# Optimization experiments

Hardware: AMD Instinct MI355X
Metric: run time of the kernel (lower is better)

The kernel has to match this reference:

```python
import jax, jax.numpy as jnp
import numpy as np

B, S, I, E, NH, HID, L = 32, 512, 64, 128, 8, 1024, 4
HD = E // NH
TEMP = 0.05
EPS_BN = 1e-5
EPS_LN = 1e-5


def _pe(seq_len, d_model):
    # sinusoidal positional encoding, matches PositionalEncoding buffer pe[:seq_len, 0, :]
    pos = jnp.arange(seq_len, dtype=jnp.float32)[:, None]
    div = jnp.exp(jnp.arange(0, d_model, 2, dtype=jnp.float32) * (-np.log(10000.0) / d_model))
    pe = jnp.zeros((seq_len, d_model), jnp.float32)
    pe = pe.at[:, 0::2].set(jnp.sin(pos * div))
    pe = pe.at[:, 1::2].set(jnp.cos(pos * div))
    return pe


def _bn(x, g, b, axis):
    # eval-mode BatchNorm1d with running_mean=0, running_var=1 (affine scale+shift)
    sh = [1] * x.ndim
    sh[axis] = -1
    return x * (g / jnp.sqrt(1.0 + EPS_BN)).reshape(sh) + b.reshape(sh)


def _ln(x, g, b):
    m = jnp.mean(x, axis=-1, keepdims=True)
    v = jnp.var(x, axis=-1, keepdims=True)
    return (x - m) / jnp.sqrt(v + EPS_LN) * g + b


def _layer(h, Wqkv, bqkv, Wo, bo, g1, b1, g2, b2, W1, bf1, W2, bf2):
    # h: (S, B, E); post-LN torch TransformerEncoderLayer, relu FFN
    s, b = h.shape[0], h.shape[1]
    qkv = h @ Wqkv + bqkv                                  # (S, B, 3E)
    q, k, v = jnp.split(qkv, 3, axis=-1)
    sp = lambda t: t.reshape(s, b, NH, HD).transpose(1, 2, 0, 3)  # (B, NH, S, HD)
    q, k, v = sp(q), sp(k), sp(v)
    att = jax.nn.softmax(jnp.einsum('bhqd,bhkd->bhqk', q, k) * (1.0 / np.sqrt(HD)), axis=-1)
    o = jnp.einsum('bhqk,bhkd->bhqd', att, v).transpose(2, 0, 1, 3).reshape(s, b, E)
    h = _ln(h + o @ Wo + bo, g1, b1)
    ff = jax.nn.relu(h @ W1 + bf1) @ W2 + bf2
    h = _ln(h + ff, g2, b2)
    return h, att.mean(axis=1)  # attn averaged over heads: (B, S, S)


def setup_inputs() -> dict:
    key = jax.random.key(0)
    ks = iter(jax.random.split(key, 64))
    r = lambda *sh: jax.random.normal(next(ks), sh, jnp.float32) * 0.02
    return dict(
        x=jax.random.normal(next(ks), (B, S, I), jnp.float32),
        Wt=r(I, E), bt=r(E),
        bn1_g=jnp.ones(E), bn1_b=jnp.zeros(E),
        bn2_g=jnp.ones(E), bn2_b=jnp.zeros(E),
        Wqkv=r(L, E, 3 * E), bqkv=r(L, 3 * E), Wo=r(L, E, E), bo=r(L, E),
        ln1_g=jnp.ones((L, E)), ln1_b=jnp.zeros((L, E)),
        ln2_g=jnp.ones((L, E)), ln2_b=jnp.zeros((L, E)),
        W1=r(L, E, HID), b1=r(L, HID), W2=r(L, HID, E), b2=r(L, E),
        bn3_g=jnp.ones(E), bn3_b=jnp.zeros(E),
        Wd=r(E, I), bd=r(I), bn4_g=jnp.ones(I), bn4_b=jnp.zeros(I),
        Ws=r(S, HID), bs=r(HID), bn5_g=jnp.ones(HID), bn5_b=jnp.zeros(HID),
        Wtext=r(1024, HID), btext=r(HID), lnT_g=jnp.ones(HID), lnT_b=jnp.zeros(HID),
        sensor_emb=jax.random.normal(next(ks), (I, 1024), jnp.float32),
    )


def reference(x, Wt, bt, bn1_g, bn1_b, bn2_g, bn2_b,
              Wqkv, bqkv, Wo, bo, ln1_g, ln1_b, ln2_g, ln2_b,
              W1, b1, W2, b2, bn3_g, bn3_b,
              Wd, bd, bn4_g, bn4_b, Ws, bs, bn5_g, bn5_b,
              Wtext, btext, lnT_g, lnT_b, sensor_emb):
    # trunk_net: Linear -> BN(E) -> PE -> BN(E)
    h = x @ Wt + bt                                  # (B, S, E)
    h = _bn(h.transpose(0, 2, 1), bn1_g, bn1_b, 1)   # (B, E, S)
    h = h.transpose(2, 0, 1)                         # (S, B, E)
    h = h + _pe(h.shape[0], E)[:, None, :]
    h = _bn(h.transpose(1, 2, 0), bn2_g, bn2_b, 1)   # (B, E, S)
    h = h.transpose(2, 0, 1)                         # (S, B, E)
    for i in range(L):
        h, attn = _layer(h, Wqkv[i], bqkv[i], Wo[i], bo[i],
                         ln1_g[i], ln1_b[i], ln2_g[i], ln2_b[i],
                         W1[i], b1[i], W2[i], b2[i])
    h = _bn(h.transpose(1, 2, 0), bn3_g, bn3_b, 1)   # (B, E, S)
    # downsample_embedding_to_input_net
    d = jax.nn.relu(h.transpose(0, 2, 1) @ Wd + bd)  # (B, S, I)
    d = _bn(d.transpose(0, 2, 1), bn4_g, bn4_b, 1)   # (B, I, S)
    # sequence_representation_net
    imu = jax.nn.relu(d @ Ws + bs)                   # (B, I, HID)
    imu = _bn(imu, bn5_g, bn5_b, 2)
    # text_to_shared_net on sensor embeddings
    sens = _ln(jax.nn.relu(sensor_emb @ Wtext + btext), lnT_g, lnT_b)  # (I, HID)
    # fused pairwise cosine similarity (torch expands to (B,I,I,HID); we don't)
    imu_n = imu / jnp.maximum(jnp.linalg.norm(imu, axis=-1, keepdims=True), 1e-8)
    sens_n = sens / jnp.maximum(jnp.linalg.norm(sens, axis=-1, keepdims=True), 1e-8)
    return jnp.einsum('bih,jh->bij', imu_n, sens_n) / TEMP  # (B, I, I)
```

## Files before the change

kernel.cpp:

```cpp
#include <hip/hip_runtime.h>
#include <hip/hip_bf16.h>

#define B_   32
#define S_   512
#define I_   64
#define E_   128
#define NH_  8
#define HD_  16
#define HID_ 1024
#define L_   4
#define NTOK (B_*S_)

typedef __hip_bfloat16 bf16;
typedef __attribute__((ext_vector_type(8))) short bf16x8;
typedef __attribute__((ext_vector_type(4))) short bf16x4;
typedef __attribute__((ext_vector_type(4))) float f32x4;

__device__ __forceinline__ float b2f(bf16 v) { return __bfloat162float(v); }

template<bool F32>
__device__ __forceinline__ float ld(const void* p, size_t i) {
    if (F32) return ((const float*)p)[i];
    return b2f(((const bf16*)p)[i]);
}

__device__ __forceinline__ unsigned short f2bu(float f) {
    union { bf16 h; unsigned short u; } c; c.h = __float2bfloat16(f); return c.u;
}
__device__ __forceinline__ unsigned short b2u(bf16 h) {
    union { bf16 h; unsigned short u; } c; c.h = h; return c.u;
}
__device__ __forceinline__ float u2f(unsigned short u) {
    return __uint_as_float((unsigned int)u << 16);
}

__global__ void k_flag(const void* bn1g, int* flag) {
    if (threadIdx.x == 0) {
        const unsigned short* u = (const unsigned short*)bn1g;
        int zeros = 0;
        for (int i = 0; i < 32; ++i) zeros += (u[i] == 0);
        flag[0] = (zeros >= 8) ? 1 : 0;
    }
}

template<bool F32>
__device__ void tr_body(const void* in, bf16* __restrict__ out, int R, int C,
                        float (*tile)[33])
{
    size_t off = (size_t)blockIdx.z * R * C;
    int c0 = blockIdx.x * 32, r0 = blockIdx.y * 32;
    int tx = threadIdx.x;
    for (int i = threadIdx.y; i < 32; i += 8)
        tile[i][tx] = ld<F32>(in, off + (size_t)(r0 + i) * C + c0 + tx);
    __syncthreads();
    for (int i = threadIdx.y; i < 32; i += 8)
        out[off + (size_t)(c0 + i) * R + r0 + tx] = __float2bfloat16(tile[tx][i]);
}
__global__ __launch_bounds__(256) void k_tr(
    const void* in, bf16* out, int R, int C, const int* flag)
{
    __shared__ float tile[32][33];
    if (*flag) tr_body<true>(in, out, R, C, tile);
    else       tr_body<false>(in, out, R, C, tile);
}

template<bool F32>
__device__ void trunk_body(const void* x, const void* Wt, const void* bt,
                           const void* g1, const void* c1,
                           const void* g2, const void* c2, float* __restrict__ h,
                           float (*xs)[I_])
{
    const int TOK = 8;
    int t0 = blockIdx.x * TOK;
    int tid = threadIdx.x;
    for (int idx = tid; idx < TOK * I_; idx += 128) {
        int tt = idx >> 6, k = idx & 63;
        xs[tt][k] = ld<F32>(x, (size_t)(t0 + tt) * I_ + k);
    }
    __syncthreads();
    int e = tid;
    float acc[TOK];
    float bias = ld<F32>(bt, e);
#pragma unroll
    for (int tt = 0; tt < TOK; ++tt) acc[tt] = bias;
    for (int k = 0; k < I_; ++k) {
        float w = ld<F32>(Wt, k * E_ + e);
#pragma unroll
        for (int tt = 0; tt < TOK; ++tt) acc[tt] += xs[tt][k] * w;
    }
    float rs = rsqrtf(1.0f + 1e-5f);
    float a1 = ld<F32>(g1, e) * rs, d1 = ld<F32>(c1, e);
    float a2 = ld<F32>(g2, e) * rs, d2 = ld<F32>(c2, e);
    int p = e >> 1;
    float freq = __expf(-(float)p * 0.14391157f);
#pragma unroll
    for (int tt = 0; tt < TOK; ++tt) {
        int t = t0 + tt;
        int s = t & (S_ - 1);
        float ang = (float)s * freq;
        float pe = (e & 1) ? cosf(ang) : sinf(ang);
        float v = acc[tt] * a1 + d1 + pe;
        h[(size_t)t * E_ + e] = v * a2 + d2;
    }
}
__global__ __launch_bounds__(128) void k_trunk(
    const void* x, const void* Wt, const void* bt,
    const void* g1, const void* c1, const void* g2, const void* c2,
    float* h, const int* flag)
{
    __shared__ float xs[8][I_];
    if (*flag) trunk_body<true>(x, Wt, bt, g1, c1, g2, c2, h, xs);
    else       trunk_body<false>(x, Wt, bt, g1, c1, g2, c2, h, xs);
}

template<bool F32>
__device__ void qkvm_body(const float* __restrict__ h, const bf16* __restrict__ WT,
                          const void* bias, size_t obi, bf16* __restrict__ qkv,
                          unsigned short (*A_s)[136])
{
    int t0 = blockIdx.x * 32;
    int tid = threadIdx.x;
    int wv = tid >> 6, lane = tid & 63;
    int l15 = lane & 15, quad = lane >> 4;

    {
        const float4* h4 = (const float4*)(h + (size_t)t0 * E_);
        for (int i = tid; i < 32 * E_ / 4; i += 256) {
            float4 v = h4[i];
            int row = i >> 5, col = (i & 31) * 4;
            A_s[row][col + 0] = f2bu(v.x);
            A_s[row][col + 1] = f2bu(v.y);
            A_s[row][col + 2] = f2bu(v.z);
            A_s[row][col + 3] = f2bu(v.w);
        }
    }
    __syncthreads();

    bf16x8 af[2][4];
#pragma unroll
    for (int kt = 0; kt < 4; ++kt) {
        int k0 = kt * 32 + quad * 8;
        af[0][kt] = *(const bf16x8*)&A_s[l15][k0];
        af[1][kt] = *(const bf16x8*)&A_s[16 + l15][k0];
    }
    for (int nt = 0; nt < 6; ++nt) {
        int col = wv * 96 + nt * 16 + l15;
        f32x4 acc0 = {0.f, 0.f, 0.f, 0.f}, acc1 = {0.f, 0.f, 0.f, 0.f};
#pragma unroll
        for (int kt = 0; kt < 4; ++kt) {
            bf16x8 bfr = *(const bf16x8*)&WT[(size_t)col * E_ + kt * 32 + quad * 8];
            acc0 = __builtin_amdgcn_mfma_f32_16x16x32_bf16(af[0][kt], bfr, acc0, 0, 0, 0);
            acc1 = __builtin_amdgcn_mfma_f32_16x16x32_bf16(af[1][kt], bfr, acc1, 0, 0, 0);
        }
        float bb = ld<F32>(bias, obi + col);
#pragma unroll
        for (int r = 0; r < 4; ++r) {
            qkv[(size_t)(t0 + quad * 4 + r) * 384 + col]      = __float2bfloat16(acc0[r] + bb);
            qkv[(size_t)(t0 + 16 + quad * 4 + r) * 384 + col] = __float2bfloat16(acc1[r] + bb);
        }
    }
}
__global__ __launch_bounds__(256) void k_qkv(
    const float* h, const bf16* WT, const void* bias, size_t obi,
    bf16* qkv, const int* flag)
{
    __shared__ unsigned short A_s[32][136];
    if (*flag) qkvm_body<true>(h, WT, bias, obi, qkv, A_s);
    else       qkvm_body<false>(h, WT, bias, obi, qkv, A_s);
}

__global__ __launch_bounds__(512) void k_attn(bf16* qkv)
{
    __shared__ unsigned short Ks[S_ * 16];
    __shared__ unsigned short Qs[256 * 16];
    __shared__ unsigned short VT[HD_ * 520];

    int bx = blockIdx.x;
    int qh = bx & 1;
    int hh = (bx >> 1) & (NH_ - 1);
    int b  = bx >> 4;
    int tid = threadIdx.x;
    const size_t base = (size_t)(b * S_) * 384 + hh * HD_;
    const float qs = 0.25f * 1.44269504f;

    for (int i = tid; i < S_ * 2; i += 512) {
        int s = i >> 1, hf = i & 1;
        uint4 v = *(const uint4*)(qkv + base + (size_t)s * 384 + 128 + hf * 8);
        unsigned int* w = (unsigned int*)&v;
#pragma unroll
        for (int j = 0; j < 4; ++j) {
            unsigned int lo = f2bu(u2f((unsigned short)(w[j] & 0xffff)) * qs);
            unsigned int hi = f2bu(u2f((unsigned short)(w[j] >> 16)) * qs);
            w[j] = lo | (hi << 16);
        }
        *(uint4*)&Ks[s * 16 + hf * 8] = v;
    }
    for (int i = tid; i < 256 * 2; i += 512) {
        int s = i >> 1, hf = i & 1;
        *(uint4*)&Qs[s * 16 + hf * 8] =
            *(const uint4*)(qkv + base + (size_t)(qh * 256 + s) * 384 + hf * 8);
    }
    {
        int s = tid;
        uint4 v0 = *(const uint4*)(qkv + base + (size_t)s * 384 + 256);
        uint4 v1 = *(const uint4*)(qkv + base + (size_t)s * 384 + 256 + 8);
        const unsigned short* u0 = (const unsigned short*)&v0;
        const unsigned short* u1 = (const unsigned short*)&v1;
#pragma unroll
        for (int dd = 0; dd < 8; ++dd) VT[dd * 520 + s] = u0[dd];
#pragma unroll
        for (int dd = 0; dd < 8; ++dd) VT[(8 + dd) * 520 + s] = u1[dd];
    }
    __syncthreads();

    int wv = tid >> 6, lane = tid & 63;
    int l15 = lane & 15, quad = lane >> 4;
    const f32x4 z4 = {0.f, 0.f, 0.f, 0.f};

    bf16x4 bq0 = *(const bf16x4*)&Qs[(wv * 32 + l15) * 16 + quad * 4];
    bf16x4 bq1 = *(const bf16x4*)&Qs[(wv * 32 + 16 + l15) * 16 + quad * 4];

    f32x4 O0 = z4, O1 = z4;
    float den0 = 0.f, den1 = 0.f;

#pragma unroll 2
    for (int kt = 0; kt < 32; ++kt) {
        bf16x4 ak = *(const bf16x4*)&Ks[(kt * 16 + l15) * 16 + quad * 4];
        bf16x4 av = *(const bf16x4*)&VT[l15 * 520 + kt * 16 + quad * 4];

        f32x4 s0 = __builtin_amdgcn_mfma_f32_16x16x16bf16_1k(ak, bq0, z4, 0, 0, 0);
        f32x4 s1 = __builtin_amdgcn_mfma_f32_16x16x16bf16_1k(ak, bq1, z4, 0, 0, 0);

        float p0[4], p1[4];
#pragma unroll
        for (int r = 0; r < 4; ++r) { p0[r] = exp2f(s0[r]); den0 += p0[r]; }
#pragma unroll
        for (int r = 0; r < 4; ++r) { p1[r] = exp2f(s1[r]); den1 += p1[r]; }

        bf16x4 pa0, pa1;
#pragma unroll
        for (int r = 0; r < 4; ++r) { pa0[r] = (short)f2bu(p0[r]); pa1[r] = (short)f2bu(p1[r]); }

        O0 = __builtin_amdgcn_mfma_f32_16x16x16bf16_1k(av, pa0, O0, 0, 0, 0);
        O1 = __builtin_amdgcn_mfma_f32_16x16x16bf16_1k(av, pa1, O1, 0, 0, 0);
    }

    den0 += __shfl_xor(den0, 16, 64);
    den0 += __shfl_xor(den0, 32, 64);
    den1 += __shfl_xor(den1, 16, 64);
    den1 += __shfl_xor(den1, 32, 64);
    float inv0 = 1.0f / den0;
    float inv1 = 1.0f / den1;

    int q0 = qh * 256 + wv * 32 + l15;
    bf16* out0 = qkv + (size_t)(b * S_ + q0) * 384 + hh * HD_ + quad * 4;
    bf16* out1 = out0 + (size_t)16 * 384;
    unsigned int a0 = (unsigned int)f2bu(O0[0] * inv0) | ((unsigned int)f2bu(O0[1] * inv0) << 16);
    unsigned int a1 = (unsigned int)f2bu(O0[2] * inv0) | ((unsigned int)f2bu(O0[3] * inv0) << 16);
    *(uint2*)out0 = (uint2){a0, a1};
    unsigned int c0 = (unsigned int)f2bu(O1[0] * inv1) | ((unsigned int)f2bu(O1[1] * inv1) << 16);
    unsigned int c1 = (unsigned int)f2bu(O1[2] * inv1) | ((unsigned int)f2bu(O1[3] * inv1) << 16);
    *(uint2*)out1 = (uint2){c0, c1};
}

template<bool F32>
__device__ void projm_body(const bf16* __restrict__ qkv, const bf16* __restrict__ WoT,
                           const void* bo, size_t obo,
                           const void* g, const void* be, size_t oln,
                           float* __restrict__ h,
                           unsigned short (*A_s)[136], float (*red)[32][2])
{
    int t0 = blockIdx.x * 32;
    int tid = threadIdx.x;
    int wv = tid >> 6, lane = tid & 63;
    int l15 = lane & 15, quad = lane >> 4;

    for (int i = tid; i < 32 * 16; i += 256) {
        int row = i >> 4, seg = i & 15;
        *(uint4*)&A_s[row][seg * 8] =
            *(const uint4*)&qkv[(size_t)(t0 + row) * 384 + seg * 8];
    }
    __syncthreads();

    bf16x8 af[2][4];
#pragma unroll
    for (int kt = 0; kt < 4; ++kt) {
        int k0 = kt * 32 + quad * 8;
        af[0][kt] = *(const bf16x8*)&A_s[l15][k0];
        af[1][kt] = *(const bf16x8*)&A_s[16 + l15][k0];
    }
    f32x4 acc[2][2];
#pragma unroll
    for (int a = 0; a < 2; ++a)
#pragma unroll
        for (int bn = 0; bn < 2; ++bn) acc[a][bn] = (f32x4){0.f, 0.f, 0.f, 0.f};
    int c0 = wv * 32 + l15, c1 = c0 + 16;
#pragma unroll
    for (int kt = 0; kt < 4; ++kt) {
        int k0 = kt * 32 + quad * 8;
        bf16x8 bb0 = *(const bf16x8*)&WoT[(size_t)c0 * E_ + k0];
        bf16x8 bb1 = *(const bf16x8*)&WoT[(size_t)c1 * E_ + k0];
        acc[0][0] = __builtin_amdgcn_mfma_f32_16x16x32_bf16(af[0][kt], bb0, acc[0][0], 0, 0, 0);
        acc[1][0] = __builtin_amdgcn_mfma_f32_16x16x32_bf16(af[1][kt], bb0, acc[1][0], 0, 0, 0);
        acc[0][1] = __builtin_amdgcn_mfma_f32_16x16x32_bf16(af[0][kt], bb1, acc[0][1], 0, 0, 0);
        acc[1][1] = __builtin_amdgcn_mfma_f32_16x16x32_bf16(af[1][kt], bb1, acc[1][1], 0, 0, 0);
    }

    float bo0 = ld<F32>(bo, obo + c0), bo1 = ld<F32>(bo, obo + c1);
    float val[2][2][4], s1[2][4], s2[2][4];
#pragma unroll
    for (int mt = 0; mt < 2; ++mt) {
#pragma unroll
        for (int r = 0; r < 4; ++r) {
            size_t row = (size_t)(t0 + mt * 16 + quad * 4 + r);
            float v0 = acc[mt][0][r] + bo0 + h[row * E_ + c0];
            float v1 = acc[mt][1][r] + bo1 + h[row * E_ + c1];
            val[mt][0][r] = v0; val[mt][1][r] = v1;
            s1[mt][r] = v0 + v1;
            s2[mt][r] = v0 * v0 + v1 * v1;
        }
    }
#pragma unroll
    for (int off = 1; off < 16; off <<= 1) {
#pragma unroll
        for (int mt = 0; mt < 2; ++mt)
#pragma unroll
            for (int r = 0; r < 4; ++r) {
                s1[mt][r] += __shfl_xor(s1[mt][r], off, 64);
                s2[mt][r] += __shfl_xor(s2[mt][r], off, 64);
            }
    }
    if (l15 == 0) {
#pragma unroll
        for (int mt = 0; mt < 2; ++mt)
#pragma unroll
            for (int r = 0; r < 4; ++r) {
                red[wv][mt * 16 + quad * 4 + r][0] = s1[mt][r];
                red[wv][mt * 16 + quad * 4 + r][1] = s2[mt][r];
            }
    }
    __syncthreads();
    float g0 = ld<F32>(g, oln + c0), g1v = ld<F32>(g, oln + c1);
    float be0 = ld<F32>(be, oln + c0), be1 = ld<F32>(be, oln + c1);
#pragma unroll
    for (int mt = 0; mt < 2; ++mt) {
#pragma unroll
        for (int r = 0; r < 4; ++r) {
            int rw = mt * 16 + quad * 4 + r;
            float su = red[0][rw][0] + red[1][rw][0] + red[2][rw][0] + red[3][rw][0];
            float sq = red[0][rw][1] + red[1][rw][1] + red[2][rw][1] + red[3][rw][1];
            float mean = su * (1.0f / E_);
            float var = fmaxf(sq * (1.0f / E_) - mean * mean, 0.0f);
            float rstd = rsqrtf(var + 1e-5f);
            size_t row = (size_t)(t0 + rw);
            h[row * E_ + c0] = (val[mt][0][r] - mean) * rstd * g0 + be0;
            h[row * E_ + c1] = (val[mt][1][r] - mean) * rstd * g1v + be1;
        }
    }
}
__global__ __launch_bounds__(256) void k_proj(
    const bf16* qkv, const bf16* WoT, const void* bo, size_t obo,
    const void* g, const void* be, size_t oln, float* h, const int* flag)
{
    __shared__ unsigned short A_s[32][136];
    __shared__ float red[4][32][2];
    if (*flag) projm_body<true>(qkv, WoT, bo, obo, g, be, oln, h, A_s, red);
    else       projm_body<false>(qkv, WoT, bo, obo, g, be, oln, h, A_s, red);
}

#define FTOK 32
#define APAD 8
#define MPAD 8

template<bool F32>
__device__ void ffn_body(float* __restrict__ h,
                         const bf16* __restrict__ W1T, const void* b1, size_t ob1,
                         const bf16* __restrict__ W2T, const void* b2v, size_t ob2,
                         const void* g, const void* be, size_t oln,
                         unsigned short (*A_s)[E_ + APAD],
                         unsigned short (*mid_s)[HID_ + MPAD],
                         float (*red)[32][2])
{
    int t0 = blockIdx.x * FTOK;
    int tid = threadIdx.x;
    int wv = tid >> 6, lane = tid & 63;
    int l15 = lane & 15, quad = lane >> 4;

    {
        const float4* h4 = (const float4*)(h + (size_t)t0 * E_);
        for (int i = tid; i < FTOK * E_ / 4; i += 256) {
            float4 v = h4[i];
            int row = i >> 5, col = (i & 31) * 4;
            A_s[row][col + 0] = f2bu(v.x);
            A_s[row][col + 1] = f2bu(v.y);
            A_s[row][col + 2] = f2bu(v.z);
            A_s[row][col + 3] = f2bu(v.w);
        }
    }
    __syncthreads();

    {
        bf16x8 af[2][4];
#pragma unroll
        for (int kt = 0; kt < 4; ++kt) {
            int k0 = kt * 32 + quad * 8;
            af[0][kt] = *(const bf16x8*)&A_s[l15][k0];
            af[1][kt] = *(const bf16x8*)&A_s[16 + l15][k0];
        }
        for (int nt = 0; nt < 16; ++nt) {
            int col = wv * 256 + nt * 16 + l15;
            f32x4 acc0 = {0.f, 0.f, 0.f, 0.f}, acc1 = {0.f, 0.f, 0.f, 0.f};
#pragma unroll
            for (int kt = 0; kt < 4; ++kt) {
                bf16x8 bfr = *(const bf16x8*)&W1T[(size_t)col * E_ + kt * 32 + quad * 8];
                acc0 = __builtin_amdgcn_mfma_f32_16x16x32_bf16(af[0][kt], bfr, acc0, 0, 0, 0);
                acc1 = __builtin_amdgcn_mfma_f32_16x16x32_bf16(af[1][kt], bfr, acc1, 0, 0, 0);
            }
            float bias = ld<F32>(b1, ob1 + col);
#pragma unroll
            for (int r = 0; r < 4; ++r) {
                mid_s[quad * 4 + r][col]      = f2bu(fmaxf(acc0[r] + bias, 0.f));
                mid_s[16 + quad * 4 + r][col] = f2bu(fmaxf(acc1[r] + bias, 0.f));
            }
        }
    }
    __syncthreads();

    f32x4 acc[2][2];
#pragma unroll
    for (int a = 0; a < 2; ++a)
#pragma unroll
        for (int bn = 0; bn < 2; ++bn) acc[a][bn] = (f32x4){0.f, 0.f, 0.f, 0.f};
    int c0 = wv * 32 + l15;
    int c1 = wv * 32 + 16 + l15;
    for (int kt = 0; kt < 32; ++kt) {
        int k0 = kt * 32 + quad * 8;
        bf16x8 a0 = *(const bf16x8*)&mid_s[l15][k0];
        bf16x8 a1 = *(const bf16x8*)&mid_s[16 + l15][k0];
        bf16x8 bb0 = *(const bf16x8*)&W2T[(size_t)c0 * HID_ + k0];
        bf16x8 bb1 = *(const bf16x8*)&W2T[(size_t)c1 * HID_ + k0];
        acc[0][0] = __builtin_amdgcn_mfma_f32_16x16x32_bf16(a0, bb0, acc[0][0], 0, 0, 0);
        acc[1][0] = __builtin_amdgcn_mfma_f32_16x16x32_bf16(a1, bb0, acc[1][0], 0, 0, 0);
        acc[0][1] = __builtin_amdgcn_mfma_f32_16x16x32_bf16(a0, bb1, acc[0][1], 0, 0, 0);
        acc[1][1] = __builtin_amdgcn_mfma_f32_16x16x32_bf16(a1, bb1, acc[1][1], 0, 0, 0);
    }

    float bo0 = ld<F32>(b2v, ob2 + c0), bo1 = ld<F32>(b2v, ob2 + c1);
    float val[2][2][4], s1[2][4], s2[2][4];
#pragma unroll
    for (int mt = 0; mt < 2; ++mt) {
#pragma unroll
        for (int r = 0; r < 4; ++r) {
            size_t row = (size_t)(t0 + mt * 16 + quad * 4 + r);
            float v0 = acc[mt][0][r] + bo0 + h[row * E_ + c0];
            float v1 = acc[mt][1][r] + bo1 + h[row * E_ + c1];
            val[mt][0][r] = v0; val[mt][1][r] = v1;
            s1[mt][r] = v0 + v1;
            s2[mt][r] = v0 * v0 + v1 * v1;
        }
    }
#pragma unroll
    for (int off = 1; off < 16; off <<= 1) {
#pragma unroll
        for (int mt = 0; mt < 2; ++mt)
#pragma unroll
            for (int r = 0; r < 4; ++r) {
                s1[mt][r] += __shfl_xor(s1[mt][r], off, 64);
                s2[mt][r] += __shfl_xor(s2[mt][r], off, 64);
            }
    }
    if (l15 == 0) {
#pragma unroll
        for (int mt = 0; mt < 2; ++mt)
#pragma unroll
            for (int r = 0; r < 4; ++r) {
                red[wv][mt * 16 + quad * 4 + r][0] = s1[mt][r];
                red[wv][mt * 16 + quad * 4 + r][1] = s2[mt][r];
            }
    }
    __syncthreads();
    float g0 = ld<F32>(g, oln + c0), g1v = ld<F32>(g, oln + c1);
    float be0 = ld<F32>(be, oln + c0), be1 = ld<F32>(be, oln + c1);
#pragma unroll
    for (int mt = 0; mt < 2; ++mt) {
#pragma unroll
        for (int r = 0; r < 4; ++r) {
            int rw = mt * 16 + quad * 4 + r;
            float su = red[0][rw][0] + red[1][rw][0] + red[2][rw][0] + red[3][rw][0];
            float sq = red[0][rw][1] + red[1][rw][1] + red[2][rw][1] + red[3][rw][1];
            float mean = su * (1.0f / E_);
            float var = fmaxf(sq * (1.0f / E_) - mean * mean, 0.0f);
            float rstd = rsqrtf(var + 1e-5f);
            size_t row = (size_t)(t0 + rw);
            h[row * E_ + c0] = (val[mt][0][r] - mean) * rstd * g0 + be0;
            h[row * E_ + c1] = (val[mt][1][r] - mean) * rstd * g1v + be1;
        }
    }
}
__global__ __launch_bounds__(256) void k_ffn_mfma(
    float* h, const bf16* W1T, const void* b1, size_t ob1,
    const bf16* W2T, const void* b2v, size_t ob2,
    const void* g, const void* be, size_t oln, const int* flag)
{
    __shared__ unsigned short A_s[FTOK][E_ + APAD];
    __shared__ unsigned short mid_s[FTOK][HID_ + MPAD];
    __shared__ float red[4][32][2];
    if (*flag) ffn_body<true>(h, W1T, b1, ob1, W2T, b2v, ob2, g, be, oln, A_s, mid_s, red);
    else       ffn_body<false>(h, W1T, b1, ob1, W2T, b2v, ob2, g, be, oln, A_s, mid_s, red);
}

template<bool F32>
__device__ void downm_body(const float* __restrict__ h, const void* g3, const void* c3,
                           const bf16* __restrict__ WdT, const void* bd,
                           const void* g4, const void* c4, float* __restrict__ d,
                           unsigned short (*A_s)[136], float* g3s, float* c3s)
{
    int t0 = blockIdx.x * 32;
    int tid = threadIdx.x;
    if (tid < E_) {
        float rs = rsqrtf(1.0f + 1e-5f);
        g3s[tid] = ld<F32>(g3, tid) * rs;
        c3s[tid] = ld<F32>(c3, tid);
    }
    __syncthreads();
    for (int i = tid; i < 32 * E_; i += 256) {
        int row = i >> 7, col = i & 127;
        A_s[row][col] = f2bu(h[(size_t)(t0 + row) * E_ + col] * g3s[col] + c3s[col]);
    }
    __syncthreads();

    int wv = tid >> 6, lane = tid & 63;
    int l15 = lane & 15, quad = lane >> 4;
    int col = wv * 16 + l15;
    f32x4 acc0 = {0.f, 0.f, 0.f, 0.f}, acc1 = {0.f, 0.f, 0.f, 0.f};
#pragma unroll
    for (int kt = 0; kt < 4; ++kt) {
        int k0 = kt * 32 + quad * 8;
        bf16x8 a0 = *(const bf16x8*)&A_s[l15][k0];
        bf16x8 a1 = *(const bf16x8*)&A_s[16 + l15][k0];
        bf16x8 bb = *(const bf16x8*)&WdT[(size_t)col * E_ + k0];
        acc0 = __builtin_amdgcn_mfma_f32_16x16x32_bf16(a0, bb, acc0, 0, 0, 0);
        acc1 = __builtin_amdgcn_mfma_f32_16x16x32_bf16(a1, bb, acc1, 0, 0, 0);
    }
    float rs = rsqrtf(1.0f + 1e-5f);
    float bb = ld<F32>(bd, col);
    float a4 = ld<F32>(g4, col) * rs, d4 = ld<F32>(c4, col);
#pragma unroll
    for (int r = 0; r < 4; ++r) {
        d[(size_t)(t0 + quad * 4 + r) * I_ + col]      = fmaxf(acc0[r] + bb, 0.f) * a4 + d4;
        d[(size_t)(t0 + 16 + quad * 4 + r) * I_ + col] = fmaxf(acc1[r] + bb, 0.f) * a4 + d4;
    }
}
__global__ __launch_bounds__(256) void k_down(
    const float* h, const void* g3, const void* c3, const bf16* WdT, const void* bd,
    const void* g4, const void* c4, float* d, const int* flag)
{
    __shared__ unsigned short A_s[32][136];
    __shared__ float g3s[E_], c3s[E_];
    if (*flag) downm_body<true>(h, g3, c3, WdT, bd, g4, c4, d, A_s, g3s, c3s);
    else       downm_body<false>(h, g3, c3, WdT, bd, g4, c4, d, A_s, g3s, c3s);
}

template<bool F32>
__device__ void imum_body(const float* __restrict__ d, const bf16* __restrict__ WsT,
                          const void* bs, const void* g5, const void* c5,
                          float* __restrict__ imu, unsigned short (*A_s)[520])
{
    int b = blockIdx.x >> 3;
    int jc = blockIdx.x & 7;
    int tid = threadIdx.x;
    int wv = tid >> 6, lane = tid & 63;
    int l15 = lane & 15, quad = lane >> 4;

    for (int idx = tid; idx < I_ * S_; idx += 256) {
        int i = idx & 63, s = idx >> 6;
        A_s[i][s] = f2bu(d[((size_t)b * S_ + s) * I_ + i]);
    }
    __syncthreads();

    float rs = rsqrtf(1.0f + 1e-5f);
    int j0 = jc * 128 + wv * 32;
    for (int nt = 0; nt < 2; ++nt) {
        int j = j0 + nt * 16 + l15;
        f32x4 acc4[4];
#pragma unroll
        for (int mt = 0; mt < 4; ++mt) acc4[mt] = (f32x4){0.f, 0.f, 0.f, 0.f};
        for (int kt = 0; kt < 16; ++kt) {
            int k0 = kt * 32 + quad * 8;
            bf16x8 bfr = *(const bf16x8*)&WsT[(size_t)j * S_ + k0];
#pragma unroll
            for (int mt = 0; mt < 4; ++mt) {
// ... 63 lines not shown
        int k0 = kt * 32 + quad * 8;
        bf16x8 a = *(const bf16x8*)&A_s[l15][k0];
        bf16x8 bb = *(const bf16x8*)&WtT[(size_t)col * HID_ + k0];
        acc = __builtin_amdgcn_mfma_f32_16x16x32_bf16(a, bb, acc, 0, 0, 0);
    }
    float bbv = ld<F32>(bt, col);
#pragma unroll
    for (int r = 0; r < 4; ++r)
        sg[(size_t)(r0 + quad * 4 + r) * HID_ + col] = fmaxf(acc[r] + bbv, 0.f);
}
__global__ __launch_bounds__(256) void k_sens_gemm(
    const void* se, const bf16* WtT, const void* bt, float* sg, const int* flag)
{
    __shared__ unsigned short A_s[16][HID_ + 8];
    if (*flag) sensg_body<true>(se, WtT, bt, sg, A_s);
    else       sensg_body<false>(se, WtT, bt, sg, A_s);
}

template<bool F32>
__device__ void sensln_body(const float* __restrict__ sg, const void* g, const void* be,
                            bf16* __restrict__ sens_b, float (*red)[2])
{
    size_t r0 = (size_t)blockIdx.x * HID_;
    int tid = threadIdx.x;
    int wv = tid >> 6, lane = tid & 63;
    float v4[4];
    float s1 = 0.f, s2 = 0.f;
#pragma unroll
    for (int c = 0; c < 4; ++c) {
        float v = sg[r0 + tid + c * 256];
        v4[c] = v;
        s1 += v; s2 += v * v;
    }
    for (int off = 32; off; off >>= 1) {
        s1 += __shfl_down(s1, off, 64);
        s2 += __shfl_down(s2, off, 64);
    }
    if (lane == 0) { red[wv][0] = s1; red[wv][1] = s2; }
    __syncthreads();
    float su = red[0][0] + red[1][0] + red[2][0] + red[3][0];
    float sq = red[0][1] + red[1][1] + red[2][1] + red[3][1];
    float mean = su * (1.0f / HID_);
    float var = fmaxf(sq * (1.0f / HID_) - mean * mean, 0.0f);
    float rstd = rsqrtf(var + 1e-5f);
    float q = 0.f;
#pragma unroll
    for (int c = 0; c < 4; ++c) {
        int col = tid + c * 256;
        v4[c] = (v4[c] - mean) * rstd * ld<F32>(g, col) + ld<F32>(be, col);
        q += v4[c] * v4[c];
    }
    for (int off = 32; off; off >>= 1) q += __shfl_down(q, off, 64);
    __syncthreads();
    if (lane == 0) red[wv][0] = q;
    __syncthreads();
    float tot = red[0][0] + red[1][0] + red[2][0] + red[3][0];
    float inv = 1.0f / fmaxf(sqrtf(fmaxf(tot, 0.f)), 1e-8f);
#pragma unroll
    for (int c = 0; c < 4; ++c)
        sens_b[r0 + tid + c * 256] = __float2bfloat16(v4[c] * inv);
}
__global__ __launch_bounds__(256) void k_sens_ln(
    const float* sg, const void* g, const void* be, bf16* sens_b, const int* flag)
{
    __shared__ float red[4][2];
    if (*flag) sensln_body<true>(sg, g, be, sens_b, red);
    else       sensln_body<false>(sg, g, be, sens_b, red);
}

template<bool F32>
__device__ void finalm_body(const float* __restrict__ imu_n, const bf16* __restrict__ sens_b,
                            void* __restrict__ out, unsigned short (*A_s)[HID_ + 8])
{
    int r0 = blockIdx.x * 32;
    int tid = threadIdx.x;
    int wv = tid >> 6, lane = tid & 63;
    int l15 = lane & 15, quad = lane >> 4;

    {
        const float4* i4 = (const float4*)(imu_n + (size_t)r0 * HID_);
        for (int i = tid; i < 32 * HID_ / 4; i += 256) {
            float4 v = i4[i];
            int row = i >> 8, col = (i & 255) * 4;
            A_s[row][col + 0] = f2bu(v.x);
            A_s[row][col + 1] = f2bu(v.y);
            A_s[row][col + 2] = f2bu(v.z);
            A_s[row][col + 3] = f2bu(v.w);
        }
    }
    __syncthreads();

    int j = wv * 16 + l15;
    f32x4 acc[2];
    acc[0] = (f32x4){0.f, 0.f, 0.f, 0.f};
    acc[1] = (f32x4){0.f, 0.f, 0.f, 0.f};
    for (int kt = 0; kt < 32; ++kt) {
        int k0 = kt * 32 + quad * 8;
        bf16x8 bfr = *(const bf16x8*)&sens_b[(size_t)j * HID_ + k0];
        bf16x8 a0 = *(const bf16x8*)&A_s[l15][k0];
        bf16x8 a1 = *(const bf16x8*)&A_s[16 + l15][k0];
        acc[0] = __builtin_amdgcn_mfma_f32_16x16x32_bf16(a0, bfr, acc[0], 0, 0, 0);
        acc[1] = __builtin_amdgcn_mfma_f32_16x16x32_bf16(a1, bfr, acc[1], 0, 0, 0);
    }
#pragma unroll
    for (int mt = 0; mt < 2; ++mt) {
#pragma unroll
        for (int r = 0; r < 4; ++r) {
            size_t row = (size_t)(r0 + mt * 16 + quad * 4 + r);
            float v = acc[mt][r] * 20.0f;
            if (F32) ((float*)out)[row * I_ + j] = v;
            else     ((bf16*)out)[row * I_ + j] = __float2bfloat16(v);
        }
    }
}
__global__ __launch_bounds__(256) void k_final(
    const float* imu_n, const bf16* sens_b, void* out, const int* flag)
{
    __shared__ unsigned short A_s[32][HID_ + 8];
    if (*flag) finalm_body<true>(imu_n, sens_b, out, A_s);
    else       finalm_body<false>(imu_n, sens_b, out, A_s);
}

extern "C" void kernel_launch(void* const* d_in, const int* in_sizes, int n_in,
                              void* d_out, int out_size, void* d_ws, size_t ws_size,
                              hipStream_t stream) {
    (void)in_sizes; (void)n_in; (void)out_size; (void)ws_size;
    const void* x      = d_in[0];
    const void* Wt     = d_in[1];
    const void* bt     = d_in[2];
    const void* bn1_g  = d_in[3];
    const void* bn1_b  = d_in[4];
    const void* bn2_g  = d_in[5];
    const void* bn2_b  = d_in[6];
    const void* Wqkv   = d_in[7];
    const void* bqkv   = d_in[8];
    const void* Wo     = d_in[9];
    const void* bo     = d_in[10];
    const void* ln1_g  = d_in[11];
    const void* ln1_b  = d_in[12];
    const void* ln2_g  = d_in[13];
    const void* ln2_b  = d_in[14];
    const void* W1     = d_in[15];
    const void* b1     = d_in[16];
    const void* W2     = d_in[17];
    const void* b2     = d_in[18];
    const void* bn3_g  = d_in[19];
    const void* bn3_b  = d_in[20];
    const void* Wd     = d_in[21];
    const void* bd     = d_in[22];
    const void* bn4_g  = d_in[23];
    const void* bn4_b  = d_in[24];
    const void* Wsr    = d_in[25];
    const void* bs     = d_in[26];
    const void* bn5_g  = d_in[27];
    const void* bn5_b  = d_in[28];
    const void* Wtext  = d_in[29];
    const void* btext  = d_in[30];
    const void* lnT_g  = d_in[31];
    const void* lnT_b  = d_in[32];
    const void* semb   = d_in[33];

    char* ws = (char*)d_ws;
    float* h    = (float*)(ws);
    bf16*  qkvb = (bf16*) (ws + ((size_t)8  << 20));
    float* dbuf = (float*)(ws + ((size_t)8  << 20));
    float* imu  = (float*)(ws + ((size_t)12 << 20));
    bf16*  wb   = (bf16*) (ws + ((size_t)20 << 20));
    bf16*  WqkvT = wb;
    bf16*  WoT   = wb + 196608;
    bf16*  W1T   = wb + 262144;
    bf16*  W2T   = wb + 786432;
    bf16*  WsT   = wb + 1310720;
    bf16*  sensb = wb + 1835008;
    bf16*  WdT   = wb + 1900544;
    float* sg    = (float*)(wb + 1908736);
    bf16*  WtxT  = (bf16*)ws;
    int*   flag  = (int*)  (ws + ((size_t)24 << 20));

    k_flag<<<1, 64, 0, stream>>>(bn1_g, flag);

    {
        dim3 blk(32, 8);
        k_tr<<<dim3(384/32, 128/32, L_), blk, 0, stream>>>(Wqkv, WqkvT, 128, 384, flag);
        k_tr<<<dim3(128/32, 128/32, L_), blk, 0, stream>>>(Wo,   WoT,   128, 128, flag);
        k_tr<<<dim3(1024/32, 128/32, L_), blk, 0, stream>>>(W1,  W1T,   128, 1024, flag);
        k_tr<<<dim3(128/32, 1024/32, L_), blk, 0, stream>>>(W2,  W2T,   1024, 128, flag);
        k_tr<<<dim3(1024/32, 512/32, 1), blk, 0, stream>>>(Wsr,  WsT,   512, 1024, flag);
        k_tr<<<dim3(64/32, 128/32, 1),   blk, 0, stream>>>(Wd,   WdT,   128, 64,  flag);
    }

    k_trunk<<<NTOK / 8, 128, 0, stream>>>(x, Wt, bt, bn1_g, bn1_b, bn2_g, bn2_b, h, flag);

    for (int l = 0; l < L_; ++l) {
        size_t obqkv = (size_t)l * 384;
        size_t obo   = (size_t)l * E_;
        size_t ob1   = (size_t)l * HID_;
        size_t ob2   = (size_t)l * E_;
        size_t oln   = (size_t)l * E_;
        k_qkv<<<NTOK / 32, 256, 0, stream>>>(h, WqkvT + (size_t)l * 49152,
                                             bqkv, obqkv, qkvb, flag);
        k_attn<<<B_ * NH_ * 2, 512, 0, stream>>>(qkvb);
        k_proj<<<NTOK / 32, 256, 0, stream>>>(qkvb, WoT + (size_t)l * 16384,
                                              bo, obo, ln1_g, ln1_b, oln, h, flag);
        k_ffn_mfma<<<NTOK / FTOK, 256, 0, stream>>>(h, W1T + (size_t)l * 131072, b1, ob1,
                                                    W2T + (size_t)l * 131072, b2, ob2,
                                                    ln2_g, ln2_b, oln, flag);
    }

    k_down<<<NTOK / 32, 256, 0, stream>>>(h, bn3_g, bn3_b, WdT, bd, bn4_g, bn4_b, dbuf, flag);
    {
        dim3 blk(32, 8);
        k_tr<<<dim3(1024/32, 1024/32, 1), blk, 0, stream>>>(Wtext, WtxT, 1024, 1024, flag);
    }
    k_imu<<<B_ * 8, 256, 0, stream>>>(dbuf, WsT, bs, bn5_g, bn5_b, imu, flag);
    k_norm<<<B_ * I_, 256, 0, stream>>>(imu);
    k_sens_gemm<<<64, 256, 0, stream>>>(semb, WtxT, btext, sg, flag);
    k_sens_ln<<<I_, 256, 0, stream>>>(sg, lnT_g, lnT_b, sensb, flag);
    k_final<<<(B_ * I_) / 32, 256, 0, stream>>>(imu, sensb, d_out, flag);
}
```

Before: 555.5 us.

## Fuse attention projection with FFN and batch all weight transposes into one launch

Merges the output-projection+LN1 kernel with the FFN+LN2 kernel, so the post-LN1 activations stay in registers and shared memory instead of being written to and re-read from global h. All seven weight-transpose launches are combined into one job-table kernel, and the Wtext transpose gets its own workspace slot. Several shared-memory staging loops now pack bf16 pairs into a single 8-byte store. The fused kernel holds more live registers across phases, which could lower occupancy.

```diff
diff --git a/kernel.cpp b/kernel.cpp
--- a/kernel.cpp
+++ b/kernel.cpp
@@ -43,12 +43,33 @@
     }
 }
 
-template<bool F32>
-__device__ void tr_body(const void* in, bf16* __restrict__ out, int R, int C,
-                        float (*tile)[33])
-{
-    size_t off = (size_t)blockIdx.z * R * C;
-    int c0 = blockIdx.x * 32, r0 = blockIdx.y * 32;
+struct TrJobs {
+    const void* in[7];
+    bf16*       out[7];
+    int R[7];
+    int C[7];
+    int start[8];
+};
+
+template<bool F32>
+__device__ void tr_all_body(const TrJobs& j, float (*tile)[33])
+{
+    int bid = blockIdx.x;
+    int job = 0;
+#pragma unroll
+    for (int t = 0; t < 6; ++t) if (bid >= j.start[t + 1]) job = t + 1;
+    int local = bid - j.start[job];
+    int R = j.R[job], C = j.C[job];
+    int nx = C >> 5, ny = R >> 5;
+    int per_z = nx * ny;
+    int z = local / per_z;
+    int rem = local - z * per_z;
+    int cy = rem / nx, cx = rem - cy * nx;
+    const void* in = j.in[job];
+    bf16* out = j.out[job];
+
+    size_t off = (size_t)z * R * C;
+    int c0 = cx * 32, r0 = cy * 32;
     int tx = threadIdx.x;
     for (int i = threadIdx.y; i < 32; i += 8)
         tile[i][tx] = ld<F32>(in, off + (size_t)(r0 + i) * C + c0 + tx);
@@ -56,12 +77,11 @@
     for (int i = threadIdx.y; i < 32; i += 8)
         out[off + (size_t)(c0 + i) * R + r0 + tx] = __float2bfloat16(tile[tx][i]);
 }
-__global__ __launch_bounds__(256) void k_tr(
-    const void* in, bf16* out, int R, int C, const int* flag)
+__global__ __launch_bounds__(256) void k_tr_all(TrJobs j, const int* flag)
 {
     __shared__ float tile[32][33];
-    if (*flag) tr_body<true>(in, out, R, C, tile);
-    else       tr_body<false>(in, out, R, C, tile);
+    if (*flag) tr_all_body<true>(j, tile);
+    else       tr_all_body<false>(j, tile);
 }
 
 template<bool F32>
@@ -128,10 +148,9 @@
         for (int i = tid; i < 32 * E_ / 4; i += 256) {
             float4 v = h4[i];
             int row = i >> 5, col = (i & 31) * 4;
-            A_s[row][col + 0] = f2bu(v.x);
-            A_s[row][col + 1] = f2bu(v.y);
-            A_s[row][col + 2] = f2bu(v.z);
-            A_s[row][col + 3] = f2bu(v.w);
+            unsigned int w0 = (unsigned int)f2bu(v.x) | ((unsigned int)f2bu(v.y) << 16);
+            unsigned int w1 = (unsigned int)f2bu(v.z) | ((unsigned int)f2bu(v.w) << 16);
+            *(uint2*)&A_s[row][col] = (uint2){w0, w1};
         }
     }
     __syncthreads();
@@ -263,17 +282,27 @@
     *(uint2*)out1 = (uint2){c0, c1};
 }
 
-template<bool F32>
-__device__ void projm_body(const bf16* __restrict__ qkv, const bf16* __restrict__ WoT,
-                           const void* bo, size_t obo,
-                           const void* g, const void* be, size_t oln,
-                           float* __restrict__ h,
-                           unsigned short (*A_s)[136], float (*red)[32][2])
-{
-    int t0 = blockIdx.x * 32;
+#define FTOK 32
+#define APAD 8
+#define MPAD 8
+
+template<bool F32>
+__device__ void projffn_body(const bf16* __restrict__ qkv, const bf16* __restrict__ WoT,
+                             const void* bo, size_t obo,
+                             const void* g1, const void* be1,
+                             const bf16* __restrict__ W1T, const void* b1, size_t ob1,
+                             const bf16* __restrict__ W2T, const void* b2v, size_t ob2,
+                             const void* g2, const void* be2, size_t oln,
+                             float* __restrict__ h,
+                             unsigned short (*A_s)[E_ + APAD],
+                             unsigned short (*mid_s)[HID_ + MPAD],
+                             float (*red)[32][2])
+{
+    int t0 = blockIdx.x * FTOK;
     int tid = threadIdx.x;
     int wv = tid >> 6, lane = tid & 63;
     int l15 = lane & 15, quad = lane >> 4;
+    int c0 = wv * 32 + l15, c1 = c0 + 16;
 
     for (int i = tid; i < 32 * 16; i += 256) {
         int row = i >> 4, seg = i & 15;
@@ -294,7 +323,6 @@
     for (int a = 0; a < 2; ++a)
 #pragma unroll
         for (int bn = 0; bn < 2; ++bn) acc[a][bn] = (f32x4){0.f, 0.f, 0.f, 0.f};
-    int c0 = wv * 32 + l15, c1 = c0 + 16;
 #pragma unroll
     for (int kt = 0; kt < 4; ++kt) {
         int k0 = kt * 32 + quad * 8;
@@ -340,8 +368,109 @@
             }
     }
     __syncthreads();
-    float g0 = ld<F32>(g, oln + c0), g1v = ld<F32>(g, oln + c1);
-    float be0 = ld<F32>(be, oln + c0), be1 = ld<F32>(be, oln + c1);
+
+    float val1[2][2][4];
+    {
+        float g10 = ld<F32>(g1, oln + c0), g11 = ld<F32>(g1, oln + c1);
+        float b10 = ld<F32>(be1, oln + c0), b11 = ld<F32>(be1, oln + c1);
+#pragma unroll
+        for (int mt = 0; mt < 2; ++mt) {
+#pragma unroll
+            for (int r = 0; r < 4; ++r) {
+                int rw = mt * 16 + quad * 4 + r;
+                float su = red[0][rw][0] + red[1][rw][0] + red[2][rw][0] + red[3][rw][0];
+                float sq = red[0][rw][1] + red[1][rw][1] + red[2][rw][1] + red[3][rw][1];
+                float mean = su * (1.0f / E_);
+                float var = fmaxf(sq * (1.0f / E_) - mean * mean, 0.0f);
+                float rstd = rsqrtf(var + 1e-5f);
+                float h0 = (val[mt][0][r] - mean) * rstd * g10 + b10;
+                float h1v = (val[mt][1][r] - mean) * rstd * g11 + b11;
+                val1[mt][0][r] = h0; val1[mt][1][r] = h1v;
+                A_s[rw][c0] = f2bu(h0);
+                A_s[rw][c1] = f2bu(h1v);
+            }
+        }
+    }
+    __syncthreads();
+
+    {
+        bf16x8 af1[2][4];
+#pragma unroll
+        for (int kt = 0; kt < 4; ++kt) {
+            int k0 = kt * 32 + quad * 8;
+            af1[0][kt] = *(const bf16x8*)&A_s[l15][k0];
+            af1[1][kt] = *(const bf16x8*)&A_s[16 + l15][k0];
+        }
+        for (int nt = 0; nt < 16; ++nt) {
+            int col = wv * 256 + nt * 16 + l15;
+            f32x4 acc0 = {0.f, 0.f, 0.f, 0.f}, acc1 = {0.f, 0.f, 0.f, 0.f};
+#pragma unroll
+            for (int kt = 0; kt < 4; ++kt) {
+                bf16x8 bfr = *(const bf16x8*)&W1T[(size_t)col * E_ + kt * 32 + quad * 8];
+                acc0 = __builtin_amdgcn_mfma_f32_16x16x32_bf16(af1[0][kt], bfr, acc0, 0, 0, 0);
+                acc1 = __builtin_amdgcn_mfma_f32_16x16x32_bf16(af1[1][kt], bfr, acc1, 0, 0, 0);
+            }
+            float bias = ld<F32>(b1, ob1 + col);
+#pragma unroll
+            for (int r = 0; r < 4; ++r) {
+                mid_s[quad * 4 + r][col]      = f2bu(fmaxf(acc0[r] + bias, 0.f));
+                mid_s[16 + quad * 4 + r][col] = f2bu(fmaxf(acc1[r] + bias, 0.f));
+            }
+        }
+    }
+    __syncthreads();
+
+    f32x4 acc2[2][2];
+#pragma unroll
+    for (int a = 0; a < 2; ++a)
+#pragma unroll
+        for (int bn = 0; bn < 2; ++bn) acc2[a][bn] = (f32x4){0.f, 0.f, 0.f, 0.f};
+    for (int kt = 0; kt < 32; ++kt) {
+        int k0 = kt * 32 + quad * 8;
+        bf16x8 a0 = *(const bf16x8*)&mid_s[l15][k0];
+        bf16x8 a1 = *(const bf16x8*)&mid_s[16 + l15][k0];
+        bf16x8 bb0 = *(const bf16x8*)&W2T[(size_t)c0 * HID_ + k0];
+        bf16x8 bb1 = *(const bf16x8*)&W2T[(size_t)c1 * HID_ + k0];
+        acc2[0][0] = __builtin_amdgcn_mfma_f32_16x16x32_bf16(a0, bb0, acc2[0][0], 0, 0, 0);
+        acc2[1][0] = __builtin_amdgcn_mfma_f32_16x16x32_bf16(a1, bb0, acc2[1][0], 0, 0, 0);
+        acc2[0][1] = __builtin_amdgcn_mfma_f32_16x16x32_bf16(a0, bb1, acc2[0][1], 0, 0, 0);
+        acc2[1][1] = __builtin_amdgcn_mfma_f32_16x16x32_bf16(a1, bb1, acc2[1][1], 0, 0, 0);
+    }
+
+    float b20 = ld<F32>(b2v, ob2 + c0), b21 = ld<F32>(b2v, ob2 + c1);
+#pragma unroll
+    for (int mt = 0; mt < 2; ++mt) {
+#pragma unroll
+        for (int r = 0; r < 4; ++r) {
+            float v0 = acc2[mt][0][r] + b20 + val1[mt][0][r];
+            float v1 = acc2[mt][1][r] + b21 + val1[mt][1][r];
+            val[mt][0][r] = v0; val[mt][1][r] = v1;
+            s1[mt][r] = v0 + v1;
+            s2[mt][r] = v0 * v0 + v1 * v1;
+        }
+    }
+#pragma unroll
+    for (int off = 1; off < 16; off <<= 1) {
+#pragma unroll
+        for (int mt = 0; mt < 2; ++mt)
+#pragma unroll
+            for (int r = 0; r < 4; ++r) {
+                s1[mt][r] += __shfl_xor(s1[mt][r], off, 64);
+                s2[mt][r] += __shfl_xor(s2[mt][r], off, 64);
+            }
+    }
+    if (l15 == 0) {
+#pragma unroll
+        for (int mt = 0; mt < 2; ++mt)
+#pragma unroll
+            for (int r = 0; r < 4; ++r) {
+                red[wv][mt * 16 + quad * 4 + r][0] = s1[mt][r];
+                red[wv][mt * 16 + quad * 4 + r][1] = s2[mt][r];
+            }
+    }
+    __syncthreads();
+    float g20 = ld<F32>(g2, oln + c0), g21 = ld<F32>(g2, oln + c1);
+    float be20 = ld<F32>(be2, oln + c0), be21 = ld<F32>(be2, oln + c1);
 #pragma unroll
     for (int mt = 0; mt < 2; ++mt) {
 #pragma unroll
@@ -353,160 +482,25 @@
             float var = fmaxf(sq * (1.0f / E_) - mean * mean, 0.0f);
             float rstd = rsqrtf(var + 1e-5f);
             size_t row = (size_t)(t0 + rw);
-            h[row * E_ + c0] = (val[mt][0][r] - mean) * rstd * g0 + be0;
-            h[row * E_ + c1] = (val[mt][1][r] - mean) * rstd * g1v + be1;
-        }
-    }
-}
-__global__ __launch_bounds__(256) void k_proj(
+            h[row * E_ + c0] = (val[mt][0][r] - mean) * rstd * g20 + be20;
+            h[row * E_ + c1] = (val[mt][1][r] - mean) * rstd * g21 + be21;
+        }
+    }
+}
+__global__ __launch_bounds__(256) void k_projffn(
     const bf16* qkv, const bf16* WoT, const void* bo, size_t obo,
-    const void* g, const void* be, size_t oln, float* h, const int* flag)
-{
-    __shared__ unsigned short A_s[32][136];
-    __shared__ float red[4][32][2];
-    if (*flag) projm_body<true>(qkv, WoT, bo, obo, g, be, oln, h, A_s, red);
-    else       projm_body<false>(qkv, WoT, bo, obo, g, be, oln, h, A_s, red);
-}
-
-#define FTOK 32
-#define APAD 8
-#define MPAD 8
-
-template<bool F32>
-__device__ void ffn_body(float* __restrict__ h,
-                         const bf16* __restrict__ W1T, const void* b1, size_t ob1,
-                         const bf16* __restrict__ W2T, const void* b2v, size_t ob2,
-                         const void* g, const void* be, size_t oln,
-                         unsigned short (*A_s)[E_ + APAD],
-                         unsigned short (*mid_s)[HID_ + MPAD],
-                         float (*red)[32][2])
-{
-    int t0 = blockIdx.x * FTOK;
-    int tid = threadIdx.x;
-    int wv = tid >> 6, lane = tid & 63;
-    int l15 = lane & 15, quad = lane >> 4;
-
-    {
-        const float4* h4 = (const float4*)(h + (size_t)t0 * E_);
-        for (int i = tid; i < FTOK * E_ / 4; i += 256) {
-            float4 v = h4[i];
-            int row = i >> 5, col = (i & 31) * 4;
-            A_s[row][col + 0] = f2bu(v.x);
-            A_s[row][col + 1] = f2bu(v.y);
-            A_s[row][col + 2] = f2bu(v.z);
-            A_s[row][col + 3] = f2bu(v.w);
-        }
-    }
-    __syncthreads();
-
-    {
-        bf16x8 af[2][4];
-#pragma unroll
-        for (int kt = 0; kt < 4; ++kt) {
-            int k0 = kt * 32 + quad * 8;
-            af[0][kt] = *(const bf16x8*)&A_s[l15][k0];
-            af[1][kt] = *(const bf16x8*)&A_s[16 + l15][k0];
-        }
-        for (int nt = 0; nt < 16; ++nt) {
-            int col = wv * 256 + nt * 16 + l15;
-            f32x4 acc0 = {0.f, 0.f, 0.f, 0.f}, acc1 = {0.f, 0.f, 0.f, 0.f};
-#pragma unroll
-            for (int kt = 0; kt < 4; ++kt) {
-                bf16x8 bfr = *(const bf16x8*)&W1T[(size_t)col * E_ + kt * 32 + quad * 8];
-                acc0 = __builtin_amdgcn_mfma_f32_16x16x32_bf16(af[0][kt], bfr, acc0, 0, 0, 0);
-                acc1 = __builtin_amdgcn_mfma_f32_16x16x32_bf16(af[1][kt], bfr, acc1, 0, 0, 0);
-            }
-            float bias = ld<F32>(b1, ob1 + col);
-#pragma unroll
-            for (int r = 0; r < 4; ++r) {
-                mid_s[quad * 4 + r][col]      = f2bu(fmaxf(acc0[r] + bias, 0.f));
-                mid_s[16 + quad * 4 + r][col] = f2bu(fmaxf(acc1[r] + bias, 0.f));
-            }
-        }
-    }
-    __syncthreads();
-
-    f32x4 acc[2][2];
-#pragma unroll
-    for (int a = 0; a < 2; ++a)
-#pragma unroll
-        for (int bn = 0; bn < 2; ++bn) acc[a][bn] = (f32x4){0.f, 0.f, 0.f, 0.f};
-    int c0 = wv * 32 + l15;
-    int c1 = wv * 32 + 16 + l15;
-    for (int kt = 0; kt < 32; ++kt) {
-        int k0 = kt * 32 + quad * 8;
-        bf16x8 a0 = *(const bf16x8*)&mid_s[l15][k0];
-        bf16x8 a1 = *(const bf16x8*)&mid_s[16 + l15][k0];
-        bf16x8 bb0 = *(const bf16x8*)&W2T[(size_t)c0 * HID_ + k0];
-        bf16x8 bb1 = *(const bf16x8*)&W2T[(size_t)c1 * HID_ + k0];
-        acc[0][0] = __builtin_amdgcn_mfma_f32_16x16x32_bf16(a0, bb0, acc[0][0], 0, 0, 0);
-        acc[1][0] = __builtin_amdgcn_mfma_f32_16x16x32_bf16(a1, bb0, acc[1][0], 0, 0, 0);
-        acc[0][1] = __builtin_amdgcn_mfma_f32_16x16x32_bf16(a0, bb1, acc[0][1], 0, 0, 0);
-        acc[1][1] = __builtin_amdgcn_mfma_f32_16x16x32_bf16(a1, bb1, acc[1][1], 0, 0, 0);
-    }
-
-    float bo0 = ld<F32>(b2v, ob2 + c0), bo1 = ld<F32>(b2v, ob2 + c1);
-    float val[2][2][4], s1[2][4], s2[2][4];
-#pragma unroll
-    for (int mt = 0; mt < 2; ++mt) {
-#pragma unroll
-        for (int r = 0; r < 4; ++r) {
-            size_t row = (size_t)(t0 + mt * 16 + quad * 4 + r);
-            float v0 = acc[mt][0][r] + bo0 + h[row * E_ + c0];
-            float v1 = acc[mt][1][r] + bo1 + h[row * E_ + c1];
-            val[mt][0][r] = v0; val[mt][1][r] = v1;
-            s1[mt][r] = v0 + v1;
-            s2[mt][r] = v0 * v0 + v1 * v1;
-        }
-    }
-#pragma unroll
-    for (int off = 1; off < 16; off <<= 1) {
-#pragma unroll
-        for (int mt = 0; mt < 2; ++mt)
-#pragma unroll
-            for (int r = 0; r < 4; ++r) {
-                s1[mt][r] += __shfl_xor(s1[mt][r], off, 64);
-                s2[mt][r] += __shfl_xor(s2[mt][r], off, 64);
-            }
-    }
-    if (l15 == 0) {
-#pragma unroll
-        for (int mt = 0; mt < 2; ++mt)
-#pragma unroll
-            for (int r = 0; r < 4; ++r) {
-                red[wv][mt * 16 + quad * 4 + r][0] = s1[mt][r];
-                red[wv][mt * 16 + quad * 4 + r][1] = s2[mt][r];
-            }
-    }
-    __syncthreads();
-    float g0 = ld<F32>(g, oln + c0), g1v = ld<F32>(g, oln + c1);
-    float be0 = ld<F32>(be, oln + c0), be1 = ld<F32>(be, oln + c1);
-#pragma unroll
-    for (int mt = 0; mt < 2; ++mt) {
-#pragma unroll
-        for (int r = 0; r < 4; ++r) {
-            int rw = mt * 16 + quad * 4 + r;
-            float su = red[0][rw][0] + red[1][rw][0] + red[2][rw][0] + red[3][rw][0];
-            float sq = red[0][rw][1] + red[1][rw][1] + red[2][rw][1] + red[3][rw][1];
-            float mean = su * (1.0f / E_);
-            float var = fmaxf(sq * (1.0f / E_) - mean * mean, 0.0f);
-            float rstd = rsqrtf(var + 1e-5f);
-            size_t row = (size_t)(t0 + rw);
-            h[row * E_ + c0] = (val[mt][0][r] - mean) * rstd * g0 + be0;
-            h[row * E_ + c1] = (val[mt][1][r] - mean) * rstd * g1v + be1;
-        }
-    }
-}
-__global__ __launch_bounds__(256) void k_ffn_mfma(
-    float* h, const bf16* W1T, const void* b1, size_t ob1,
+    const void* g1, const void* be1,
+    const bf16* W1T, const void* b1, size_t ob1,
     const bf16* W2T, const void* b2v, size_t ob2,
-    const void* g, const void* be, size_t oln, const int* flag)
+    const void* g2, const void* be2, size_t oln, float* h, const int* flag)
 {
     __shared__ unsigned short A_s[FTOK][E_ + APAD];
     __shared__ unsigned short mid_s[FTOK][HID_ + MPAD];
     __shared__ float red[4][32][2];
-    if (*flag) ffn_body<true>(h, W1T, b1, ob1, W2T, b2v, ob2, g, be, oln, A_s, mid_s, red);
-    else       ffn_body<false>(h, W1T, b1, ob1, W2T, b2v, ob2, g, be, oln, A_s, mid_s, red);
+    if (*flag) projffn_body<true>(qkv, WoT, bo, obo, g1, be1, W1T, b1, ob1,
+                                  W2T, b2v, ob2, g2, be2, oln, h, A_s, mid_s, red);
+    else       projffn_body<false>(qkv, WoT, bo, obo, g1, be1, W1T, b1, ob1,
+                                   W2T, b2v, ob2, g2, be2, oln, h, A_s, mid_s, red);
 }
 
 template<bool F32>
@@ -736,10 +730,9 @@
         for (int i = tid; i < 32 * HID_ / 4; i += 256) {
             float4 v = i4[i];
             int row = i >> 8, col = (i & 255) * 4;
-            A_s[row][col + 0] = f2bu(v.x);
-            A_s[row][col + 1] = f2bu(v.y);
-            A_s[row][col + 2] = f2bu(v.z);
-            A_s[row][col + 3] = f2bu(v.w);
+            unsigned int w0 = (unsigned int)f2bu(v.x) | ((unsigned int)f2bu(v.y) << 16);
+            unsigned int w1 = (unsigned int)f2bu(v.z) | ((unsigned int)f2bu(v.w) << 16);
+            *(uint2*)&A_s[row][col] = (uint2){w0, w1};
         }
     }
     __syncthreads();
@@ -828,19 +821,23 @@
     bf16*  sensb = wb + 1835008;
     bf16*  WdT   = wb + 1900544;
     float* sg    = (float*)(wb + 1908736);
-    bf16*  WtxT  = (bf16*)ws;
     int*   flag  = (int*)  (ws + ((size_t)24 << 20));
+    bf16*  WtxT  = (bf16*) (ws + ((size_t)25 << 20));
 
     k_flag<<<1, 64, 0, stream>>>(bn1_g, flag);
 
     {
-        dim3 blk(32, 8);
-        k_tr<<<dim3(384/32, 128/32, L_), blk, 0, stream>>>(Wqkv, WqkvT, 128, 384, flag);
-        k_tr<<<dim3(128/32, 128/32, L_), blk, 0, stream>>>(Wo,   WoT,   128, 128, flag);
-        k_tr<<<dim3(1024/32, 128/32, L_), blk, 0, stream>>>(W1,  W1T,   128, 1024, flag);
-        k_tr<<<dim3(128/32, 1024/32, L_), blk, 0, stream>>>(W2,  W2T,   1024, 128, flag);
-        k_tr<<<dim3(1024/32, 512/32, 1), blk, 0, stream>>>(Wsr,  WsT,   512, 1024, flag);
-        k_tr<<<dim3(64/32, 128/32, 1),   blk, 0, stream>>>(Wd,   WdT,   128, 64,  flag);
+        TrJobs tj;
+        tj.in[0] = Wqkv;  tj.out[0] = WqkvT; tj.R[0] = 128;  tj.C[0] = 384;
+        tj.in[1] = Wo;    tj.out[1] = WoT;   tj.R[1] = 128;  tj.C[1] = 128;
+        tj.in[2] = W1;    tj.out[2] = W1T;   tj.R[2] = 128;  tj.C[2] = 1024;
+        tj.in[3] = W2;    tj.out[3] = W2T;   tj.R[3] = 1024; tj.C[3] = 128;
+        tj.in[4] = Wsr;   tj.out[4] = WsT;   tj.R[4] = 512;  tj.C[4] = 1024;
+        tj.in[5] = Wd;    tj.out[5] = WdT;   tj.R[5] = 128;  tj.C[5] = 64;
+        tj.in[6] = Wtext; tj.out[6] = WtxT;  tj.R[6] = 1024; tj.C[6] = 1024;
+        const int st[8] = {0, 192, 256, 768, 1280, 1792, 1800, 2824};
+        for (int i = 0; i < 8; ++i) tj.start[i] = st[i];
+        k_tr_all<<<2824, dim3(32, 8), 0, stream>>>(tj, flag);
     }
 
     k_trunk<<<NTOK / 8, 128, 0, stream>>>(x, Wt, bt, bn1_g, bn1_b, bn2_g, bn2_b, h, flag);
@@ -854,18 +851,14 @@
         k_qkv<<<NTOK / 32, 256, 0, stream>>>(h, WqkvT + (size_t)l * 49152,
                                              bqkv, obqkv, qkvb, flag);
         k_attn<<<B_ * NH_ * 2, 512, 0, stream>>>(qkvb);
-        k_proj<<<NTOK / 32, 256, 0, stream>>>(qkvb, WoT + (size_t)l * 16384,
-                                              bo, obo, ln1_g, ln1_b, oln, h, flag);
-        k_ffn_mfma<<<NTOK / FTOK, 256, 0, stream>>>(h, W1T + (size_t)l * 131072, b1, ob1,
-                                                    W2T + (size_t)l * 131072, b2, ob2,
-                                                    ln2_g, ln2_b, oln, flag);
+        k_projffn<<<NTOK / 32, 256, 0, stream>>>(qkvb, WoT + (size_t)l * 16384, bo, obo,
+                                                 ln1_g, ln1_b,
+                                                 W1T + (size_t)l * 131072, b1, ob1,
+                                                 W2T + (size_t)l * 131072, b2, ob2,
+                                                 ln2_g, ln2_b, oln, h, flag);
     }
 
     k_down<<<NTOK / 32, 256, 0, stream>>>(h, bn3_g, bn3_b, WdT, bd, bn4_g, bn4_b, dbuf, flag);
-    {
-        dim3 blk(32, 8);
-        k_tr<<<dim3(1024/32, 1024/32, 1), blk, 0, stream>>>(Wtext, WtxT, 1024, 1024, flag);
-    }
     k_imu<<<B_ * 8, 256, 0, stream>>>(dbuf, WsT, bs, bn5_g, bn5_b, imu, flag);
     k_norm<<<B_ * I_, 256, 0, stream>>>(imu);
     k_sens_gemm<<<64, 256, 0, stream>>>(semb, WtxT, btext, sg, flag);
```

Result: faster. 520.8 us (-6.2%).
